# Performance work log

Hardware: AMD Instinct MI355X
Metric: run time of the kernel (lower is better)

## Reference

```python
import jax, jax.numpy as jnp
import numpy as np
from functools import partial

H = 64  # hidden_size
F = 5   # num_features
ALPHA_RANK = 1.0
NEG_SLOPE = 0.2


def setup_inputs() -> dict:
    key = jax.random.key(0)
    ks = jax.random.split(key, 10)
    N, T = 4096, 512
    feature = jax.random.normal(ks[0], (N, T, F), dtype=jnp.float32)
    ret = jax.random.normal(ks[1], (N,), dtype=jnp.float32)
    mask = jax.random.bernoulli(ks[2], 0.9, (N,))
    s = 1.0 / np.sqrt(H)
    Wih = jax.random.uniform(ks[3], (4 * H, F), jnp.float32, -s, s)
    Whh = jax.random.uniform(ks[4], (4 * H, H), jnp.float32, -s, s)
    bih = jax.random.uniform(ks[5], (4 * H,), jnp.float32, -s, s)
    bhh = jax.random.uniform(ks[6], (4 * H,), jnp.float32, -s, s)
    Wd = jax.random.uniform(ks[7], (1, H), jnp.float32, -s, s)
    bd = jax.random.uniform(ks[8], (1,), jnp.float32, -s, s)
    return {"feature": feature, "ret": ret, "mask": mask,
            "Wih": Wih, "Whh": Whh, "bih": bih, "bhh": bhh,
            "Wd": Wd, "bd": bd}


def _lstm_last_h(x, Wih, Whh, bih, bhh):
    # x: [N, T, F] -> last hidden state [N, H]. PyTorch gate order: i, f, g, o.
    N = x.shape[0]
    b = bih + bhh
    # precompute input projections for all steps: [T, N, 4H]
    x_proj = jnp.einsum('ntf,gf->tng', x, Wih) + b

    def step(carry, xt):
        h, c = carry
        gates = xt + h @ Whh.T  # [N, 4H]
        i, f, g, o = jnp.split(gates, 4, axis=-1)
        i = jax.nn.sigmoid(i)
        f = jax.nn.sigmoid(f)
        g = jnp.tanh(g)
        o = jax.nn.sigmoid(o)
        c = f * c + i * g
        h = o * jnp.tanh(c)
        return (h, c), None

    h0 = jnp.zeros((N, H), x.dtype)
    c0 = jnp.zeros((N, H), x.dtype)
    (h, _), _ = jax.lax.scan(step, (h0, c0), x_proj)
    return h


def _masked_mse(pred, gt, mask):
    m = mask.astype(pred.dtype)
    return jnp.sum((pred - gt) ** 2 * m) / (jnp.sum(m) + 1e-8)


def _rank_loss(pred, gt, mask):
    m = mask.astype(pred.dtype)
    pred_diff = pred[None, :] - pred[:, None]   # [i,j] = pred[j]-pred[i]
    true_diff = gt[None, :] - gt[:, None]
    mm = m[None, :] * m[:, None]
    return jnp.mean(jax.nn.relu(-pred_diff * true_diff * mm))


def reference(feature, ret, mask, Wih, Whh, bih, bhh, Wd, bd):
    h_last = _lstm_last_h(feature, Wih, Whh, bih, bhh)          # [N, H]
    pred = jax.nn.leaky_relu(h_last @ Wd.T + bd, NEG_SLOPE)[:, 0]  # [N]
    reg_loss = _masked_mse(pred, ret, mask)
    rank_loss = _rank_loss(pred, ret, mask)
    loss = reg_loss + ALPHA_RANK * rank_loss
    return pred, loss, reg_loss, rank_loss
```

## Files before the change

kernel.cpp:

```cpp
#include <hip/hip_runtime.h>

#define NSEQ   4096
#define TSTEPS 512
#define FIN    5
#define HID    64
#define SPB    16
#define BLK    256

typedef __attribute__((ext_vector_type(8))) short bsh8;
typedef __attribute__((ext_vector_type(4))) float f32x4;

#define MFMA16(A, B, C) __builtin_amdgcn_mfma_f32_16x16x32_bf16((A), (B), (C), 0, 0, 0)

struct Frag2 { bsh8 hi; bsh8 lo; };

__device__ __forceinline__ unsigned short bf16hi_rn(float x) {
    unsigned u = __float_as_uint(x);
    return (unsigned short)((u + 0x7fffu + ((u >> 16) & 1u)) >> 16);
}
__device__ __forceinline__ void split_bf16(float v, unsigned short& h, unsigned short& l) {
    h = bf16hi_rn(v);
    float hf = __uint_as_float(((unsigned)h) << 16);
    l = bf16hi_rn(v - hf);
}

__device__ __forceinline__ float fast_sigmoid(float x) {
    return __builtin_amdgcn_rcpf(1.0f + __expf(-x));
}
__device__ __forceinline__ float fast_tanh(float x) {
    return 1.0f - 2.0f * __builtin_amdgcn_rcpf(1.0f + __expf(2.0f * x));
}

__device__ __forceinline__ Frag2 load_whh_frag(const float* __restrict__ Whh, int gate, int k) {
    const float* p = Whh + gate * HID + k;
    Frag2 r;
#pragma unroll
    for (int j = 0; j < 8; ++j) {
        unsigned short h, l;
        split_bf16(p[j], h, l);
        r.hi[j] = (short)h; r.lo[j] = (short)l;
    }
    return r;
}
__device__ __forceinline__ Frag2 load_wih_frag(const float* __restrict__ Wih, int gate, int quad) {
    Frag2 r;
#pragma unroll
    for (int j = 0; j < 8; ++j) { r.hi[j] = 0; r.lo[j] = 0; }
    if (quad == 0) {
#pragma unroll
        for (int j = 0; j < FIN; ++j) {
            unsigned short h, l;
            split_bf16(Wih[gate * FIN + j], h, l);
            r.hi[j] = (short)h; r.lo[j] = (short)l;
        }
    }
    return r;
}

__device__ __forceinline__ void stage_chunk(const float* __restrict__ feat,
                                            bsh8 (*dst)[SPB],
                                            int seq0, int t0, int tid) {
#pragma unroll
    for (int it = 0; it < (64 * SPB) / BLK; ++it) {
        int idx = tid + it * BLK;
        int t2  = idx >> 4;
        int s   = idx & 15;
        const float* xp = feat + (size_t)(seq0 + s) * (TSTEPS * FIN) + (t0 + t2) * FIN;
        bsh8 v = {0, 0, 0, 0, 0, 0, 0, 0};
#pragma unroll
        for (int j = 0; j < FIN; ++j) v[j] = (short)bf16hi_rn(xp[j]);
        dst[t2][s] = v;
    }
}

__global__ __launch_bounds__(BLK)
void lstm_kernel(const float* __restrict__ feat,
                 const float* __restrict__ Wih,
                 const float* __restrict__ Whh,
                 const float* __restrict__ bih,
                 const float* __restrict__ bhh,
                 const float* __restrict__ Wd,
                 const float* __restrict__ bd,
                 float* __restrict__ pred,
                 float* __restrict__ accums) {
    __shared__ bsh8  aA[2][SPB][9];
    __shared__ bsh8  xb[2][64][SPB];
    __shared__ float hf[SPB][HID + 1];
    __shared__ float pf[SPB][17];

    const int tid  = threadIdx.x;
    const int w    = tid >> 6;
    const int lane = tid & 63;
    const int col  = lane & 15;
    const int quad = lane >> 4;
    const int u    = 16 * w + col;
    const int seq0 = blockIdx.x * SPB;

    if (blockIdx.x == 0 && tid < 4) accums[tid] = 0.0f;

    const int g0 = 0 * HID + u, g1 = 1 * HID + u, g2 = 2 * HID + u, g3 = 3 * HID + u;
    Frag2 b00 = load_whh_frag(Whh, g0, quad * 8);
    Frag2 b01 = load_whh_frag(Whh, g0, 32 + quad * 8);
    Frag2 b02 = load_wih_frag(Wih, g0, quad);
    Frag2 b10 = load_whh_frag(Whh, g1, quad * 8);
    Frag2 b11 = load_whh_frag(Whh, g1, 32 + quad * 8);
    Frag2 b12 = load_wih_frag(Wih, g1, quad);
    Frag2 b20 = load_whh_frag(Whh, g2, quad * 8);
    Frag2 b21 = load_whh_frag(Whh, g2, 32 + quad * 8);
    Frag2 b22 = load_wih_frag(Wih, g2, quad);
    Frag2 b30 = load_whh_frag(Whh, g3, quad * 8);
    Frag2 b31 = load_whh_frag(Whh, g3, 32 + quad * 8);
    Frag2 b32 = load_wih_frag(Wih, g3, quad);

    const float bi  = bih[g0] + bhh[g0];
    const float bf_ = bih[g1] + bhh[g1];
    const float bg  = bih[g2] + bhh[g2];
    const float bo  = bih[g3] + bhh[g3];

    {
        bsh8 z = {0, 0, 0, 0, 0, 0, 0, 0};
        if (tid < SPB * 9) (&aA[0][0][0])[tid] = z;
    }
    stage_chunk(feat, xb[0], seq0, 0, tid);
    __syncthreads();

    f32x4 acc0 = {bi,  bi,  bi,  bi };
    f32x4 acc1 = {bf_, bf_, bf_, bf_};
    f32x4 acc2 = {bg,  bg,  bg,  bg };
    f32x4 acc3 = {bo,  bo,  bo,  bo };
    {
        bsh8 ax = xb[0][0][col];
        acc0 = MFMA16(ax, b02.hi, acc0); acc0 = MFMA16(ax, b02.lo, acc0);
        acc1 = MFMA16(ax, b12.hi, acc1); acc1 = MFMA16(ax, b12.lo, acc1);
        acc2 = MFMA16(ax, b22.hi, acc2); acc2 = MFMA16(ax, b22.lo, acc2);
        acc3 = MFMA16(ax, b32.hi, acc3); acc3 = MFMA16(ax, b32.lo, acc3);
    }

    float c_[4] = {0.f, 0.f, 0.f, 0.f};

    for (int t = 0; t < TSTEPS; ++t) {
        const int tt  = t & 63;
        const int buf = t & 1;
        const int nb  = buf ^ 1;
        __syncthreads();

        if (tt == 0 && t + 64 < TSTEPS) {
            int nc = (t >> 6) + 1;
            stage_chunk(feat, xb[nc & 1], seq0, nc * 64, tid);
        }

        bsh8 ah0 = aA[buf][col][quad];
        bsh8 ah1 = aA[buf][col][4 + quad];
        acc0 = MFMA16(ah0, b00.hi, acc0); acc0 = MFMA16(ah1, b01.hi, acc0);
        acc1 = MFMA16(ah0, b10.hi, acc1); acc1 = MFMA16(ah1, b11.hi, acc1);
        acc2 = MFMA16(ah0, b20.hi, acc2); acc2 = MFMA16(ah1, b21.hi, acc2);
        acc3 = MFMA16(ah0, b30.hi, acc3); acc3 = MFMA16(ah1, b31.hi, acc3);
        acc0 = MFMA16(ah0, b00.lo, acc0); acc0 = MFMA16(ah1, b01.lo, acc0);
        acc1 = MFMA16(ah0, b10.lo, acc1); acc1 = MFMA16(ah1, b11.lo, acc1);
        acc2 = MFMA16(ah0, b20.lo, acc2); acc2 = MFMA16(ah1, b21.lo, acc2);
        acc3 = MFMA16(ah0, b30.lo, acc3); acc3 = MFMA16(ah1, b31.lo, acc3);

#pragma unroll
        for (int r = 0; r < 4; ++r) {
            float gi = fast_sigmoid(acc0[r]);
            float gf = fast_sigmoid(acc1[r]);
            float gg = fast_tanh  (acc2[r]);
            float go = fast_sigmoid(acc3[r]);
            c_[r] = gf * c_[r] + gi * gg;
            float hh = go * fast_tanh(c_[r]);
            int seqr = quad * 4 + r;
            ((unsigned short*)&aA[nb][seqr][0])[u] = bf16hi_rn(hh);
            if (t == TSTEPS - 1) hf[seqr][u] = hh;
        }

        if (t < TSTEPS - 1) {
            int t1 = t + 1;
            bsh8 ax = xb[(t1 >> 6) & 1][t1 & 63][col];
            acc0 = (f32x4){bi,  bi,  bi,  bi };
            acc1 = (f32x4){bf_, bf_, bf_, bf_};
            acc2 = (f32x4){bg,  bg,  bg,  bg };
            acc3 = (f32x4){bo,  bo,  bo,  bo };
            acc0 = MFMA16(ax, b02.hi, acc0); acc0 = MFMA16(ax, b02.lo, acc0);
            acc1 = MFMA16(ax, b12.hi, acc1); acc1 = MFMA16(ax, b12.lo, acc1);
            acc2 = MFMA16(ax, b22.hi, acc2); acc2 = MFMA16(ax, b22.lo, acc2);
            acc3 = MFMA16(ax, b32.hi, acc3); acc3 = MFMA16(ax, b32.lo, acc3);
        }
    }
    __syncthreads();

    {
        int s  = tid & 15;
        int q4 = tid >> 4;
        int j0 = q4 * 4;
        float part = hf[s][j0] * Wd[j0] + hf[s][j0 + 1] * Wd[j0 + 1]
                   + hf[s][j0 + 2] * Wd[j0 + 2] + hf[s][j0 + 3] * Wd[j0 + 3];
        pf[s][q4] = part;
    }
    __syncthreads();
    if (tid < SPB) {
        float sum = bd[0];
#pragma unroll
        for (int j = 0; j < 16; ++j) sum += pf[tid][j];
        float p = (sum >= 0.0f) ? sum : 0.2f * sum;
        pred[seq0 + tid] = p;
    }
}

__global__ __launch_bounds__(256)
void loss_kernel(const float* __restrict__ pred,
                 const float* __restrict__ ret,
                 const int* __restrict__ mask,
                 float* __restrict__ accums) {
    __shared__ float sp[NSEQ];
    __shared__ float sg[NSEQ];
    __shared__ float sq[NSEQ];
    int tid = threadIdx.x;
    for (int idx = tid; idx < NSEQ; idx += 256) {
        sp[idx] = pred[idx];
        sg[idx] = ret[idx];
        sq[idx] = (mask[idx] != 0) ? 1.0f : 0.0f;
    }
    __syncthreads();

    if (blockIdx.x == 0) {
        float v = 0.0f, m = 0.0f;
        for (int j = tid; j < NSEQ; j += 256) {
            float mj = sq[j];
            float d  = sp[j] - sg[j];
            v += d * d * mj;
            m += mj;
        }
#pragma unroll
        for (int off = 32; off > 0; off >>= 1) {
            v += __shfl_down(v, off, 64);
            m += __shfl_down(m, off, 64);
        }
        if ((tid & 63) == 0) {
            atomicAdd(&accums[0], v);
            atomicAdd(&accums[1], m);
        }
    }

    int iloc = tid >> 4;
    int jp   = tid & 15;
    int i    = blockIdx.x * 16 + iloc;
    float pi = sp[i], gi = sg[i], qi = sq[i];
    float sum = 0.0f;
    for (int j = jp; j < NSEQ; j += 16) {
        float t = -(sp[j] - pi) * (sg[j] - gi);
        sum += fmaxf(t, 0.0f) * sq[j];
    }
    sum *= qi;
#pragma unroll
    for (int off = 32; off > 0; off >>= 1) sum += __shfl_down(sum, off, 64);
    __shared__ float wsum[4];
    if ((tid & 63) == 0) wsum[tid >> 6] = sum;
    __syncthreads();
    if (tid == 0) atomicAdd(&accums[2], wsum[0] + wsum[1] + wsum[2] + wsum[3]);
}

__global__ void final_kernel(const float* __restrict__ accums,
                             float* __restrict__ out) {
    float reg  = accums[0] / (accums[1] + 1e-8f);
    float rank = accums[2] / 16777216.0f;
    out[NSEQ + 0] = reg + rank;
    out[NSEQ + 1] = reg;
    out[NSEQ + 2] = rank;
}

extern "C" void kernel_launch(void* const* d_in, const int* in_sizes, int n_in,
                              void* d_out, int out_size, void* d_ws, size_t ws_size,
                              hipStream_t stream) {
    const float* feat = (const float*)d_in[0];
    const float* ret  = (const float*)d_in[1];
    const int*   mask = (const int*)d_in[2];
    const float* Wih  = (const float*)d_in[3];
    const float* Whh  = (const float*)d_in[4];
    const float* bih  = (const float*)d_in[5];
    const float* bhh  = (const float*)d_in[6];
    const float* Wd   = (const float*)d_in[7];
    const float* bd   = (const float*)d_in[8];
    float* out    = (float*)d_out;
    float* accums = (float*)d_ws;

    lstm_kernel<<<NSEQ / SPB, BLK, 0, stream>>>(feat, Wih, Whh, bih, bhh,
                                                Wd, bd, out, accums);
    loss_kernel<<<NSEQ / 16, 256, 0, stream>>>(out, ret, mask, accums);
    final_kernel<<<1, 1, 0, stream>>>(accums, out);
}
```

Measured before the change: 399.9 us.

## Split LSTM gates across two wave halves with LDS gate exchange

The block grows from 4 to 8 waves. Each half of the waves computes two of the four gate groups, so every wave runs half as many MFMAs per step. Pre-activations are exchanged through a new LDS buffer, and each wave finishes the cell update for half of the rows. This shortens the per-step MFMA chain on the serial recurrence, at the cost of a second __syncthreads per step and extra LDS traffic.

Result: slower. 508.9 us (+27.3%).

```diff
diff --git a/kernel.cpp b/kernel.cpp
--- a/kernel.cpp
+++ b/kernel.cpp
@@ -5,7 +5,7 @@
 #define FIN    5
 #define HID    64
 #define SPB    16
-#define BLK    256
+#define BLK    512
 
 typedef __attribute__((ext_vector_type(8))) short bsh8;
 typedef __attribute__((ext_vector_type(4))) float f32x4;
@@ -55,22 +55,6 @@
         }
     }
     return r;
-}
-
-__device__ __forceinline__ void stage_chunk(const float* __restrict__ feat,
-                                            bsh8 (*dst)[SPB],
-                                            int seq0, int t0, int tid) {
-#pragma unroll
-    for (int it = 0; it < (64 * SPB) / BLK; ++it) {
-        int idx = tid + it * BLK;
-        int t2  = idx >> 4;
-        int s   = idx & 15;
-        const float* xp = feat + (size_t)(seq0 + s) * (TSTEPS * FIN) + (t0 + t2) * FIN;
-        bsh8 v = {0, 0, 0, 0, 0, 0, 0, 0};
-#pragma unroll
-        for (int j = 0; j < FIN; ++j) v[j] = (short)bf16hi_rn(xp[j]);
-        dst[t2][s] = v;
-    }
 }
 
 __global__ __launch_bounds__(BLK)
@@ -85,6 +69,7 @@
                  float* __restrict__ accums) {
     __shared__ bsh8  aA[2][SPB][9];
     __shared__ bsh8  xb[2][64][SPB];
+    __shared__ float xg[4][SPB][HID + 1];
     __shared__ float hf[SPB][HID + 1];
     __shared__ float pf[SPB][17];
 
@@ -93,102 +78,124 @@
     const int lane = tid & 63;
     const int col  = lane & 15;
     const int quad = lane >> 4;
-    const int u    = 16 * w + col;
+    const int u4   = w & 3;
+    const int half = w >> 2;
+    const int u    = 16 * u4 + col;
     const int seq0 = blockIdx.x * SPB;
+    const int ro   = 2 * half;
+    const int fo   = 2 - 2 * half;
 
     if (blockIdx.x == 0 && tid < 4) accums[tid] = 0.0f;
 
-    const int g0 = 0 * HID + u, g1 = 1 * HID + u, g2 = 2 * HID + u, g3 = 3 * HID + u;
-    Frag2 b00 = load_whh_frag(Whh, g0, quad * 8);
-    Frag2 b01 = load_whh_frag(Whh, g0, 32 + quad * 8);
-    Frag2 b02 = load_wih_frag(Wih, g0, quad);
-    Frag2 b10 = load_whh_frag(Whh, g1, quad * 8);
-    Frag2 b11 = load_whh_frag(Whh, g1, 32 + quad * 8);
-    Frag2 b12 = load_wih_frag(Wih, g1, quad);
-    Frag2 b20 = load_whh_frag(Whh, g2, quad * 8);
-    Frag2 b21 = load_whh_frag(Whh, g2, 32 + quad * 8);
-    Frag2 b22 = load_wih_frag(Wih, g2, quad);
-    Frag2 b30 = load_whh_frag(Whh, g3, quad * 8);
-    Frag2 b31 = load_whh_frag(Whh, g3, 32 + quad * 8);
-    Frag2 b32 = load_wih_frag(Wih, g3, quad);
-
-    const float bi  = bih[g0] + bhh[g0];
-    const float bf_ = bih[g1] + bhh[g1];
-    const float bg  = bih[g2] + bhh[g2];
-    const float bo  = bih[g3] + bhh[g3];
+    const int gA = (2 * half + 0) * HID + u;
+    const int gB = (2 * half + 1) * HID + u;
+    Frag2 bA0 = load_whh_frag(Whh, gA, quad * 8);
+    Frag2 bA1 = load_whh_frag(Whh, gA, 32 + quad * 8);
+    Frag2 bA2 = load_wih_frag(Wih, gA, quad);
+    Frag2 bB0 = load_whh_frag(Whh, gB, quad * 8);
+    Frag2 bB1 = load_whh_frag(Whh, gB, 32 + quad * 8);
+    Frag2 bB2 = load_wih_frag(Wih, gB, quad);
+
+    const float bsA = bih[gA] + bhh[gA];
+    const float bsB = bih[gB] + bhh[gB];
 
     {
         bsh8 z = {0, 0, 0, 0, 0, 0, 0, 0};
         if (tid < SPB * 9) (&aA[0][0][0])[tid] = z;
     }
-    stage_chunk(feat, xb[0], seq0, 0, tid);
-    __syncthreads();
-
-    f32x4 acc0 = {bi,  bi,  bi,  bi };
-    f32x4 acc1 = {bf_, bf_, bf_, bf_};
-    f32x4 acc2 = {bg,  bg,  bg,  bg };
-    f32x4 acc3 = {bo,  bo,  bo,  bo };
+#pragma unroll
+    for (int it = 0; it < (64 * SPB) / BLK; ++it) {
+        int idx = tid + it * BLK;
+        int t2  = idx >> 4;
+        int s   = idx & 15;
+        const float* xp = feat + (size_t)(seq0 + s) * (TSTEPS * FIN) + t2 * FIN;
+        bsh8 v = {0, 0, 0, 0, 0, 0, 0, 0};
+#pragma unroll
+        for (int j = 0; j < FIN; ++j) v[j] = (short)bf16hi_rn(xp[j]);
+        xb[0][t2][s] = v;
+    }
+    __syncthreads();
+
+    f32x4 accA = {bsA, bsA, bsA, bsA};
+    f32x4 accB = {bsB, bsB, bsB, bsB};
     {
         bsh8 ax = xb[0][0][col];
-        acc0 = MFMA16(ax, b02.hi, acc0); acc0 = MFMA16(ax, b02.lo, acc0);
-        acc1 = MFMA16(ax, b12.hi, acc1); acc1 = MFMA16(ax, b12.lo, acc1);
-        acc2 = MFMA16(ax, b22.hi, acc2); acc2 = MFMA16(ax, b22.lo, acc2);
-        acc3 = MFMA16(ax, b32.hi, acc3); acc3 = MFMA16(ax, b32.lo, acc3);
-    }
-
-    float c_[4] = {0.f, 0.f, 0.f, 0.f};
+        accA = MFMA16(ax, bA2.hi, accA); accA = MFMA16(ax, bA2.lo, accA);
+        accB = MFMA16(ax, bB2.hi, accB); accB = MFMA16(ax, bB2.lo, accB);
+    }
+
+    float c_[2] = {0.f, 0.f};
 
     for (int t = 0; t < TSTEPS; ++t) {
         const int tt  = t & 63;
         const int buf = t & 1;
         const int nb  = buf ^ 1;
-        __syncthreads();
-
-        if (tt == 0 && t + 64 < TSTEPS) {
-            int nc = (t >> 6) + 1;
-            stage_chunk(feat, xb[nc & 1], seq0, nc * 64, tid);
-        }
 
         bsh8 ah0 = aA[buf][col][quad];
         bsh8 ah1 = aA[buf][col][4 + quad];
-        acc0 = MFMA16(ah0, b00.hi, acc0); acc0 = MFMA16(ah1, b01.hi, acc0);
-        acc1 = MFMA16(ah0, b10.hi, acc1); acc1 = MFMA16(ah1, b11.hi, acc1);
-        acc2 = MFMA16(ah0, b20.hi, acc2); acc2 = MFMA16(ah1, b21.hi, acc2);
-        acc3 = MFMA16(ah0, b30.hi, acc3); acc3 = MFMA16(ah1, b31.hi, acc3);
-        acc0 = MFMA16(ah0, b00.lo, acc0); acc0 = MFMA16(ah1, b01.lo, acc0);
-        acc1 = MFMA16(ah0, b10.lo, acc1); acc1 = MFMA16(ah1, b11.lo, acc1);
-        acc2 = MFMA16(ah0, b20.lo, acc2); acc2 = MFMA16(ah1, b21.lo, acc2);
-        acc3 = MFMA16(ah0, b30.lo, acc3); acc3 = MFMA16(ah1, b31.lo, acc3);
-
-#pragma unroll
-        for (int r = 0; r < 4; ++r) {
-            float gi = fast_sigmoid(acc0[r]);
-            float gf = fast_sigmoid(acc1[r]);
-            float gg = fast_tanh  (acc2[r]);
-            float go = fast_sigmoid(acc3[r]);
-            c_[r] = gf * c_[r] + gi * gg;
-            float hh = go * fast_tanh(c_[r]);
-            int seqr = quad * 4 + r;
-            ((unsigned short*)&aA[nb][seqr][0])[u] = bf16hi_rn(hh);
-            if (t == TSTEPS - 1) hf[seqr][u] = hh;
+        accA = MFMA16(ah0, bA0.hi, accA); accA = MFMA16(ah1, bA1.hi, accA);
+        accB = MFMA16(ah0, bB0.hi, accB); accB = MFMA16(ah1, bB1.hi, accB);
+        accA = MFMA16(ah0, bA0.lo, accA); accA = MFMA16(ah1, bA1.lo, accA);
+        accB = MFMA16(ah0, bB0.lo, accB); accB = MFMA16(ah1, bB1.lo, accB);
+
+        xg[2 * half + 0][quad * 4 + fo + 0][u] = accA[fo + 0];
+        xg[2 * half + 0][quad * 4 + fo + 1][u] = accA[fo + 1];
+        xg[2 * half + 1][quad * 4 + fo + 0][u] = accB[fo + 0];
+        xg[2 * half + 1][quad * 4 + fo + 1][u] = accB[fo + 1];
+        __syncthreads();
+
+        if (tt == 0 && t + 64 < TSTEPS) {
+            int nc  = (t >> 6) + 1;
+            int t0n = nc * 64;
+            bsh8 (*dst)[SPB] = xb[nc & 1];
+#pragma unroll
+            for (int it = 0; it < (64 * SPB) / BLK; ++it) {
+                int idx = tid + it * BLK;
+                int t2  = idx >> 4;
+                int s   = idx & 15;
+                const float* xp = feat + (size_t)(seq0 + s) * (TSTEPS * FIN)
+                                       + (t0n + t2) * FIN;
+                bsh8 v = {0, 0, 0, 0, 0, 0, 0, 0};
+#pragma unroll
+                for (int j = 0; j < FIN; ++j) v[j] = (short)bf16hi_rn(xp[j]);
+                dst[t2][s] = v;
+            }
+        }
+
+#pragma unroll
+        for (int j = 0; j < 2; ++j) {
+            const int r = ro + j;
+            const int s = quad * 4 + r;
+            float vi, vf, vg, vo;
+            if (half == 0) {
+                vi = accA[r];      vf = accB[r];
+                vg = xg[2][s][u];  vo = xg[3][s][u];
+            } else {
+                vi = xg[0][s][u];  vf = xg[1][s][u];
+                vg = accA[r];      vo = accB[r];
+            }
+            float gi = fast_sigmoid(vi);
+            float gf = fast_sigmoid(vf);
+            float gg = fast_tanh  (vg);
+            float go = fast_sigmoid(vo);
+            c_[j] = gf * c_[j] + gi * gg;
+            float hh = go * fast_tanh(c_[j]);
+            ((unsigned short*)&aA[nb][s][0])[u] = bf16hi_rn(hh);
+            if (t == TSTEPS - 1) hf[s][u] = hh;
         }
 
         if (t < TSTEPS - 1) {
             int t1 = t + 1;
             bsh8 ax = xb[(t1 >> 6) & 1][t1 & 63][col];
-            acc0 = (f32x4){bi,  bi,  bi,  bi };
-            acc1 = (f32x4){bf_, bf_, bf_, bf_};
-            acc2 = (f32x4){bg,  bg,  bg,  bg };
-            acc3 = (f32x4){bo,  bo,  bo,  bo };
-            acc0 = MFMA16(ax, b02.hi, acc0); acc0 = MFMA16(ax, b02.lo, acc0);
-            acc1 = MFMA16(ax, b12.hi, acc1); acc1 = MFMA16(ax, b12.lo, acc1);
-            acc2 = MFMA16(ax, b22.hi, acc2); acc2 = MFMA16(ax, b22.lo, acc2);
-            acc3 = MFMA16(ax, b32.hi, acc3); acc3 = MFMA16(ax, b32.lo, acc3);
-        }
-    }
-    __syncthreads();
-
-    {
+            accA = (f32x4){bsA, bsA, bsA, bsA};
+            accB = (f32x4){bsB, bsB, bsB, bsB};
+            accA = MFMA16(ax, bA2.hi, accA); accA = MFMA16(ax, bA2.lo, accA);
+            accB = MFMA16(ax, bB2.hi, accB); accB = MFMA16(ax, bB2.lo, accB);
+        }
+        __syncthreads();
+    }
+
+    if (tid < 256) {
         int s  = tid & 15;
         int q4 = tid >> 4;
         int j0 = q4 * 4;
```

## Split block into two 8-sequence groups and overlap MFMA with gate epilogue

Applied to the files above, without the earlier changes.

Splits the 16 sequences per block into two interleaved groups of 8. One group's gate matmul runs while the other group's elementwise LSTM update executes. Gate pre-activations are now written to a shared-memory buffer, so the nonlinear epilogue is spread across all 256 threads, each handling two units, instead of each MFMA lane doing four rows. The aim is to hide MFMA latency and the transcendental epilogue inside the serial recurrence. The cost is an extra shared-memory round trip, two barriers per step, and MFMAs that compute 16 rows while only 8 are used.

After: 629.9 us. 57.5% more time.

```diff
diff --git a/kernel.cpp b/kernel.cpp
--- a/kernel.cpp
+++ b/kernel.cpp
@@ -6,6 +6,7 @@
 #define HID    64
 #define SPB    16
 #define BLK    256
+#define GP     68
 
 typedef __attribute__((ext_vector_type(8))) short bsh8;
 typedef __attribute__((ext_vector_type(4))) float f32x4;
@@ -20,8 +21,8 @@
 }
 __device__ __forceinline__ void split_bf16(float v, unsigned short& h, unsigned short& l) {
     h = bf16hi_rn(v);
-    float hf = __uint_as_float(((unsigned)h) << 16);
-    l = bf16hi_rn(v - hf);
+    float hf_ = __uint_as_float(((unsigned)h) << 16);
+    l = bf16hi_rn(v - hf_);
 }
 
 __device__ __forceinline__ float fast_sigmoid(float x) {
@@ -55,22 +56,6 @@
         }
     }
     return r;
-}
-
-__device__ __forceinline__ void stage_chunk(const float* __restrict__ feat,
-                                            bsh8 (*dst)[SPB],
-                                            int seq0, int t0, int tid) {
-#pragma unroll
-    for (int it = 0; it < (64 * SPB) / BLK; ++it) {
-        int idx = tid + it * BLK;
-        int t2  = idx >> 4;
-        int s   = idx & 15;
-        const float* xp = feat + (size_t)(seq0 + s) * (TSTEPS * FIN) + (t0 + t2) * FIN;
-        bsh8 v = {0, 0, 0, 0, 0, 0, 0, 0};
-#pragma unroll
-        for (int j = 0; j < FIN; ++j) v[j] = (short)bf16hi_rn(xp[j]);
-        dst[t2][s] = v;
-    }
 }
 
 __global__ __launch_bounds__(BLK)
@@ -83,8 +68,9 @@
                  const float* __restrict__ bd,
                  float* __restrict__ pred,
                  float* __restrict__ accums) {
-    __shared__ bsh8  aA[2][SPB][9];
+    __shared__ bsh8  aG[2][2][8][9];
     __shared__ bsh8  xb[2][64][SPB];
+    __shared__ float gt[2][4][8][GP];
     __shared__ float hf[SPB][HID + 1];
     __shared__ float pf[SPB][17];
 
@@ -94,6 +80,8 @@
     const int col  = lane & 15;
     const int quad = lane >> 4;
     const int u    = 16 * w + col;
+    const int es   = tid >> 5;
+    const int eu   = tid & 31;
     const int seq0 = blockIdx.x * SPB;
 
     if (blockIdx.x == 0 && tid < 4) accums[tid] = 0.0f;
@@ -119,73 +107,113 @@
 
     {
         bsh8 z = {0, 0, 0, 0, 0, 0, 0, 0};
-        if (tid < SPB * 9) (&aA[0][0][0])[tid] = z;
-    }
-    stage_chunk(feat, xb[0], seq0, 0, tid);
-    __syncthreads();
-
-    f32x4 acc0 = {bi,  bi,  bi,  bi };
-    f32x4 acc1 = {bf_, bf_, bf_, bf_};
-    f32x4 acc2 = {bg,  bg,  bg,  bg };
-    f32x4 acc3 = {bo,  bo,  bo,  bo };
-    {
-        bsh8 ax = xb[0][0][col];
-        acc0 = MFMA16(ax, b02.hi, acc0); acc0 = MFMA16(ax, b02.lo, acc0);
-        acc1 = MFMA16(ax, b12.hi, acc1); acc1 = MFMA16(ax, b12.lo, acc1);
-        acc2 = MFMA16(ax, b22.hi, acc2); acc2 = MFMA16(ax, b22.lo, acc2);
-        acc3 = MFMA16(ax, b32.hi, acc3); acc3 = MFMA16(ax, b32.lo, acc3);
-    }
-
-    float c_[4] = {0.f, 0.f, 0.f, 0.f};
+        bsh8* p = &aG[0][0][0][0];
+        for (int i = tid; i < 2 * 2 * 8 * 9; i += BLK) p[i] = z;
+    }
+#pragma unroll
+    for (int it = 0; it < (64 * SPB) / BLK; ++it) {
+        int idx = tid + it * BLK;
+        int t2  = idx >> 4;
+        int s   = idx & 15;
+        const float* xp = feat + (size_t)(seq0 + s) * (TSTEPS * FIN) + t2 * FIN;
+        bsh8 v = {0, 0, 0, 0, 0, 0, 0, 0};
+#pragma unroll
+        for (int j = 0; j < FIN; ++j) v[j] = (short)bf16hi_rn(xp[j]);
+        xb[0][t2][s] = v;
+    }
+    __syncthreads();
+
+    f32x4 acc0, acc1, acc2, acc3;
+    float c00 = 0.f, c01 = 0.f, c10 = 0.f, c11 = 0.f;
+
+#define MSTEP(G)                                                           \
+    {                                                                      \
+        acc0 = (f32x4){bi,  bi,  bi,  bi };                                \
+        acc1 = (f32x4){bf_, bf_, bf_, bf_};                                \
+        acc2 = (f32x4){bg,  bg,  bg,  bg };                                \
+        acc3 = (f32x4){bo,  bo,  bo,  bo };                                \
+        bsh8 ax = xb[cb][tt][(G) * 8 + (col & 7)];                         \
+        acc0 = MFMA16(ax, b02.hi, acc0); acc0 = MFMA16(ax, b02.lo, acc0);  \
+        acc1 = MFMA16(ax, b12.hi, acc1); acc1 = MFMA16(ax, b12.lo, acc1);  \
+        acc2 = MFMA16(ax, b22.hi, acc2); acc2 = MFMA16(ax, b22.lo, acc2);  \
+        acc3 = MFMA16(ax, b32.hi, acc3); acc3 = MFMA16(ax, b32.lo, acc3);  \
+        bsh8 ah0 = aG[G][buf][col & 7][quad];                              \
+        bsh8 ah1 = aG[G][buf][col & 7][4 + quad];                          \
+        acc0 = MFMA16(ah0, b00.hi, acc0); acc0 = MFMA16(ah1, b01.hi, acc0);\
+        acc1 = MFMA16(ah0, b10.hi, acc1); acc1 = MFMA16(ah1, b11.hi, acc1);\
+        acc2 = MFMA16(ah0, b20.hi, acc2); acc2 = MFMA16(ah1, b21.hi, acc2);\
+        acc3 = MFMA16(ah0, b30.hi, acc3); acc3 = MFMA16(ah1, b31.hi, acc3);\
+        acc0 = MFMA16(ah0, b00.lo, acc0); acc0 = MFMA16(ah1, b01.lo, acc0);\
+        acc1 = MFMA16(ah0, b10.lo, acc1); acc1 = MFMA16(ah1, b11.lo, acc1);\
+        acc2 = MFMA16(ah0, b20.lo, acc2); acc2 = MFMA16(ah1, b21.lo, acc2);\
+        acc3 = MFMA16(ah0, b30.lo, acc3); acc3 = MFMA16(ah1, b31.lo, acc3);\
+    }
+
+#define GTWR(G)                                                            \
+    if (quad < 2) {                                                        \
+        _Pragma("unroll")                                                  \
+        for (int r = 0; r < 4; ++r) {                                      \
+            gt[G][0][quad * 4 + r][u] = acc0[r];                           \
+            gt[G][1][quad * 4 + r][u] = acc1[r];                           \
+            gt[G][2][quad * 4 + r][u] = acc2[r];                           \
+            gt[G][3][quad * 4 + r][u] = acc3[r];                           \
+        }                                                                  \
+    }
+
+#define EPILOG(G, CA, CB, DSTROW, WHF)                                     \
+    {                                                                      \
+        float vi0 = gt[G][0][es][eu],      vf0 = gt[G][1][es][eu];         \
+        float vg0 = gt[G][2][es][eu],      vo0 = gt[G][3][es][eu];         \
+        float vi1 = gt[G][0][es][eu + 32], vf1 = gt[G][1][es][eu + 32];    \
+        float vg1 = gt[G][2][es][eu + 32], vo1 = gt[G][3][es][eu + 32];    \
+        float gi0 = fast_sigmoid(vi0), gf0 = fast_sigmoid(vf0);            \
+        float gg0 = fast_tanh(vg0),    go0 = fast_sigmoid(vo0);            \
+        float gi1 = fast_sigmoid(vi1), gf1 = fast_sigmoid(vf1);            \
+        float gg1 = fast_tanh(vg1),    go1 = fast_sigmoid(vo1);            \
+        CA = gf0 * CA + gi0 * gg0;                                         \
+        CB = gf1 * CB + gi1 * gg1;                                         \
+        float hh0 = go0 * fast_tanh(CA);                                   \
+        float hh1 = go1 * fast_tanh(CB);                                   \
+        ((unsigned short*)(DSTROW))[eu]      = bf16hi_rn(hh0);             \
+        ((unsigned short*)(DSTROW))[eu + 32] = bf16hi_rn(hh1);             \
+        if (WHF) { hf[(G) * 8 + es][eu]      = hh0;                        \
+                   hf[(G) * 8 + es][eu + 32] = hh1; }                      \
+    }
 
     for (int t = 0; t < TSTEPS; ++t) {
         const int tt  = t & 63;
+        const int cb  = (t >> 6) & 1;
         const int buf = t & 1;
         const int nb  = buf ^ 1;
+
+        MSTEP(0)
+        if (t > 0) {
+            EPILOG(1, c10, c11, &aG[1][buf][es][0], false)
+        }
+        GTWR(0)
+        if (tt == 0 && t + 64 < TSTEPS) {
+            int t0n = t + 64;
+#pragma unroll
+            for (int it = 0; it < (64 * SPB) / BLK; ++it) {
+                int idx = tid + it * BLK;
+                int t2  = idx >> 4;
+                int s   = idx & 15;
+                const float* xp = feat + (size_t)(seq0 + s) * (TSTEPS * FIN)
+                                       + (t0n + t2) * FIN;
+                bsh8 v = {0, 0, 0, 0, 0, 0, 0, 0};
+#pragma unroll
+                for (int j = 0; j < FIN; ++j) v[j] = (short)bf16hi_rn(xp[j]);
+                xb[cb ^ 1][t2][s] = v;
+            }
+        }
         __syncthreads();
 
-        if (tt == 0 && t + 64 < TSTEPS) {
-            int nc = (t >> 6) + 1;
-            stage_chunk(feat, xb[nc & 1], seq0, nc * 64, tid);
-        }
-
-        bsh8 ah0 = aA[buf][col][quad];
-        bsh8 ah1 = aA[buf][col][4 + quad];
-        acc0 = MFMA16(ah0, b00.hi, acc0); acc0 = MFMA16(ah1, b01.hi, acc0);
-        acc1 = MFMA16(ah0, b10.hi, acc1); acc1 = MFMA16(ah1, b11.hi, acc1);
-        acc2 = MFMA16(ah0, b20.hi, acc2); acc2 = MFMA16(ah1, b21.hi, acc2);
-        acc3 = MFMA16(ah0, b30.hi, acc3); acc3 = MFMA16(ah1, b31.hi, acc3);
-        acc0 = MFMA16(ah0, b00.lo, acc0); acc0 = MFMA16(ah1, b01.lo, acc0);
-        acc1 = MFMA16(ah0, b10.lo, acc1); acc1 = MFMA16(ah1, b11.lo, acc1);
-        acc2 = MFMA16(ah0, b20.lo, acc2); acc2 = MFMA16(ah1, b21.lo, acc2);
-        acc3 = MFMA16(ah0, b30.lo, acc3); acc3 = MFMA16(ah1, b31.lo, acc3);
-
-#pragma unroll
-        for (int r = 0; r < 4; ++r) {
-            float gi = fast_sigmoid(acc0[r]);
-            float gf = fast_sigmoid(acc1[r]);
-            float gg = fast_tanh  (acc2[r]);
-            float go = fast_sigmoid(acc3[r]);
-            c_[r] = gf * c_[r] + gi * gg;
-            float hh = go * fast_tanh(c_[r]);
-            int seqr = quad * 4 + r;
-            ((unsigned short*)&aA[nb][seqr][0])[u] = bf16hi_rn(hh);
-            if (t == TSTEPS - 1) hf[seqr][u] = hh;
-        }
-
-        if (t < TSTEPS - 1) {
-            int t1 = t + 1;
-            bsh8 ax = xb[(t1 >> 6) & 1][t1 & 63][col];
-            acc0 = (f32x4){bi,  bi,  bi,  bi };
-            acc1 = (f32x4){bf_, bf_, bf_, bf_};
-            acc2 = (f32x4){bg,  bg,  bg,  bg };
-            acc3 = (f32x4){bo,  bo,  bo,  bo };
-            acc0 = MFMA16(ax, b02.hi, acc0); acc0 = MFMA16(ax, b02.lo, acc0);
-            acc1 = MFMA16(ax, b12.hi, acc1); acc1 = MFMA16(ax, b12.lo, acc1);
-            acc2 = MFMA16(ax, b22.hi, acc2); acc2 = MFMA16(ax, b22.lo, acc2);
-            acc3 = MFMA16(ax, b32.hi, acc3); acc3 = MFMA16(ax, b32.lo, acc3);
-        }
-    }
+        MSTEP(1)
+        EPILOG(0, c00, c01, &aG[0][nb][es][0], t == TSTEPS - 1)
+        GTWR(1)
+        __syncthreads();
+    }
+    EPILOG(1, c10, c11, &aG[1][0][es][0], true)
     __syncthreads();
 
     {
@@ -204,6 +232,9 @@
         float p = (sum >= 0.0f) ? sum : 0.2f * sum;
         pred[seq0 + tid] = p;
     }
+#undef MSTEP
+#undef GTWR
+#undef EPILOG
 }
 
 __global__ __launch_bounds__(256)
```
